# Performance work log

Hardware: AMD Instinct MI355X
Metric: run time of the kernel (lower is better)

The kernel has to match this reference:

```python
import jax, jax.numpy as jnp
import numpy as np

EPS = 1e-20

def efficient_squash(s):
    # Efficient-CapsNet squash: (1 - 1/e^||s||) * s/||s||
    n = jnp.linalg.norm(s, axis=-1, keepdims=True)
    return (1.0 - 1.0 / (jnp.exp(n) + EPS)) * (s / (n + EPS))

def setup_inputs() -> dict:
    key = jax.random.key(0)
    k1, k2 = jax.random.split(key)
    B, N, D_in = 32, 2048, 16
    K, D_out = 32, 16
    x = jax.random.normal(k1, (B, N, D_in), dtype=jnp.float32)
    # he_normal fan_in = N * D_in * ... ; use simple scaled normal init
    w = jax.random.normal(k2, (K, N, D_in, D_out), dtype=jnp.float32) * 0.05
    b = jnp.zeros((K, N, 1), dtype=jnp.float32)
    return {"x": x, "w": w, "b": b}

def reference(x, w, b):
    D_out = w.shape[-1]
    # projection: [B,N,D_in] x [K,N,D_in,D_out] -> [B,K,N,D_out]
    u = jnp.einsum('bji,kjiz->bkjz', x, w)
    # agreement c_{bkj} = sum_{i,z} u_{bkjz} u_{bkiz} = <u_j, sum_i u_i>
    t = jnp.sum(u, axis=2)                      # [B,K,D_out]
    c = jnp.einsum('bkjz,bkz->bkj', u, t)[..., None]  # [B,K,N,1]
    c = c / jnp.sqrt(jnp.asarray(D_out, jnp.float32))
    c = jax.nn.softmax(c, axis=1)               # softmax over capsules K
    c = c + b                                   # broadcast [K,N,1]
    s = jnp.sum(u * c, axis=2)                  # [B,K,D_out]
    return efficient_squash(s)
```

## Files before the change

kernel.cpp:

```cpp
#include <hip/hip_runtime.h>

#define NN 2048

typedef __attribute__((ext_vector_type(8))) short short8;
typedef __attribute__((ext_vector_type(4))) float f32x4;

#define WS_TPART 0UL
#define WS_SPART 33554432UL
#define WS_TP2   67108864UL
#define WS_SP2   68157440UL
#define WS_TG    69206016UL
#define WS_NEED  69271552UL

__device__ __forceinline__ float bf_lo(unsigned v) { return __uint_as_float(v << 16); }
__device__ __forceinline__ float bf_hi(unsigned v) { return __uint_as_float(v & 0xffff0000u); }
__device__ __forceinline__ unsigned pack_bf16(float a, float b) {
    unsigned ua = __float_as_uint(a), ub = __float_as_uint(b);
    return ((ua + 0x8000u) >> 16) | ((ub + 0x8000u) & 0xffff0000u);
}
__device__ __forceinline__ short8 pack8(const float* r) {
    short8 o;
#pragma unroll
    for (int e = 0; e < 8; ++e)
        o[e] = (short)(unsigned short)((__float_as_uint(r[e]) + 0x8000u) >> 16);
    return o;
}
__device__ __forceinline__ short8 sel8(bool keep, short8 v) {
    union { short8 s; unsigned u[4]; } a, b;
    a.s = v;
#pragma unroll
    for (int i = 0; i < 4; ++i) b.u[i] = keep ? a.u[i] : 0u;
    return b.s;
}

__device__ __forceinline__ float dpp_sum16(float v) {
    int a;
    a = __builtin_amdgcn_update_dpp(0, __float_as_int(v), 0x121, 0xf, 0xf, false);
    v += __int_as_float(a);
    a = __builtin_amdgcn_update_dpp(0, __float_as_int(v), 0x122, 0xf, 0xf, false);
    v += __int_as_float(a);
    a = __builtin_amdgcn_update_dpp(0, __float_as_int(v), 0x124, 0xf, 0xf, false);
    v += __int_as_float(a);
    a = __builtin_amdgcn_update_dpp(0, __float_as_int(v), 0x128, 0xf, 0xf, false);
    v += __int_as_float(a);
    return v;
}
__device__ __forceinline__ float dpp_max16(float v) {
    int a;
    a = __builtin_amdgcn_update_dpp(0, __float_as_int(v), 0x121, 0xf, 0xf, false);
    v = fmaxf(v, __int_as_float(a));
    a = __builtin_amdgcn_update_dpp(0, __float_as_int(v), 0x122, 0xf, 0xf, false);
    v = fmaxf(v, __int_as_float(a));
    a = __builtin_amdgcn_update_dpp(0, __float_as_int(v), 0x124, 0xf, 0xf, false);
    v = fmaxf(v, __int_as_float(a));
    a = __builtin_amdgcn_update_dpp(0, __float_as_int(v), 0x128, 0xf, 0xf, false);
    v = fmaxf(v, __int_as_float(a));
    return v;
}

__global__ __launch_bounds__(512)
void kA(const float* __restrict__ x, const float* __restrict__ w,
        float* __restrict__ t_part)
{
    const int tid = threadIdx.x;
    const int wv = tid >> 6, l = tid & 63;
    const int z = l & 15, g = l >> 4;
    const int jl = g >> 1, ih = g & 1;
    const int j0 = blockIdx.x * 4;

    f32x4 C[4][2];
#pragma unroll
    for (int ckl = 0; ckl < 4; ++ckl)
#pragma unroll
        for (int bh = 0; bh < 2; ++bh) C[ckl][bh] = (f32x4){0.f, 0.f, 0.f, 0.f};

#pragma unroll
    for (int p = 0; p < 2; ++p) {
        const int jp = j0 + p * 2 + jl;
        short8 Af[2];
#pragma unroll
        for (int bh = 0; bh < 2; ++bh) {
            const float* xp = x + ((size_t)(bh * 16 + z) * NN + jp) * 16 + ih * 8;
            float ar[8];
            float4 v0 = *reinterpret_cast<const float4*>(xp);
            float4 v1 = *reinterpret_cast<const float4*>(xp + 4);
            ar[0]=v0.x; ar[1]=v0.y; ar[2]=v0.z; ar[3]=v0.w;
            ar[4]=v1.x; ar[5]=v1.y; ar[6]=v1.z; ar[7]=v1.w;
            Af[bh] = pack8(ar);
        }
        short8 Bf[4];
#pragma unroll
        for (int ckl = 0; ckl < 4; ++ckl) {
            const int ck = wv * 4 + ckl;
            const float* wp = w + ((size_t)ck * NN + jp) * 256 + ih * 128 + z;
            float br[8];
#pragma unroll
            for (int e = 0; e < 8; ++e) br[e] = wp[e * 16];
            Bf[ckl] = pack8(br);
        }
#pragma unroll
        for (int ckl = 0; ckl < 4; ++ckl)
#pragma unroll
            for (int bh = 0; bh < 2; ++bh)
                C[ckl][bh] = __builtin_amdgcn_mfma_f32_16x16x32_bf16(
                    Af[bh], Bf[ckl], C[ckl][bh], 0, 0, 0);
    }

    float* tp = t_part + (size_t)blockIdx.x * 16384;
#pragma unroll
    for (int ckl = 0; ckl < 4; ++ckl)
#pragma unroll
        for (int bh = 0; bh < 2; ++bh)
#pragma unroll
            for (int r = 0; r < 4; ++r)
                tp[((bh * 16 + g * 4 + r) * 32 + wv * 4 + ckl) * 16 + z] =
                    C[ckl][bh][r];
}

__global__ __launch_bounds__(256)
void kred32(const float* __restrict__ src, float* __restrict__ dst)
{
    const int idx = blockIdx.x * 256 + threadIdx.x;
    const int c4 = idx & 4095, ch = idx >> 12;
    const f32x4* P = reinterpret_cast<const f32x4*>(src);
    f32x4 a0 = (f32x4){0,0,0,0}, a1 = a0, a2 = a0, a3 = a0;
#pragma unroll 2
    for (int q = 0; q < 32; q += 4) {
        a0 += P[(size_t)(ch * 32 + q + 0) * 4096 + c4];
        a1 += P[(size_t)(ch * 32 + q + 1) * 4096 + c4];
        a2 += P[(size_t)(ch * 32 + q + 2) * 4096 + c4];
        a3 += P[(size_t)(ch * 32 + q + 3) * 4096 + c4];
    }
    reinterpret_cast<f32x4*>(dst)[(size_t)ch * 4096 + c4] = (a0 + a1) + (a2 + a3);
}

__global__ __launch_bounds__(256)
void kt2(const float* __restrict__ tp2, float* __restrict__ t_g)
{
    const int c4 = blockIdx.x * 256 + threadIdx.x;
    const f32x4* P = reinterpret_cast<const f32x4*>(tp2);
    f32x4 a0 = (f32x4){0,0,0,0}, a1 = a0, a2 = a0, a3 = a0;
#pragma unroll
    for (int q = 0; q < 16; q += 4) {
        a0 += P[(size_t)(q + 0) * 4096 + c4];
        a1 += P[(size_t)(q + 1) * 4096 + c4];
        a2 += P[(size_t)(q + 2) * 4096 + c4];
        a3 += P[(size_t)(q + 3) * 4096 + c4];
    }
    f32x4 s = (a0 + a1) + (a2 + a3);
    const int b = c4 >> 7, ck = (c4 >> 2) & 31, zq = c4 & 3;
#pragma unroll
    for (int e = 0; e < 4; ++e)
        t_g[(size_t)(ck * 16 + zq * 4 + e) * 32 + b] = s[e];
}

__global__ __launch_bounds__(512)
void kB(const float* __restrict__ x, const float* __restrict__ w,
        const float* __restrict__ t_g, const float* __restrict__ bias,
        float* __restrict__ s_part)
{
    __shared__ alignas(16) unsigned t_pk[512 * 20];
    __shared__ alignas(16) float l_lds[2][32][34];
    __shared__ alignas(16) float c_lds[2][32][34];

    const int tid = threadIdx.x;
    const int wv = tid >> 6, l = tid & 63;
    const int z = l & 15, g = l >> 4;
    const int jl = g >> 1, ih = g & 1;
    const int j0 = blockIdx.x * 4;

#pragma unroll
    for (int it = 0; it < 4; ++it) {
        const int idx = it * 512 + tid;
        const int row = idx >> 2, boff = (idx & 3) * 8;
        const float4 v0 = *reinterpret_cast<const float4*>(t_g + (size_t)row * 32 + boff);
        const float4 v1 = *reinterpret_cast<const float4*>(t_g + (size_t)row * 32 + boff + 4);
        uint4 pk;
        pk.x = pack_bf16(v0.x, v0.y);
        pk.y = pack_bf16(v0.z, v0.w);
        pk.z = pack_bf16(v1.x, v1.y);
        pk.w = pack_bf16(v1.z, v1.w);
        *reinterpret_cast<uint4*>(&t_pk[row * 20 + boff / 2]) = pk;
    }
    __syncthreads();

    f32x4 S[4][2];
#pragma unroll
    for (int ckl = 0; ckl < 4; ++ckl)
#pragma unroll
        for (int bh = 0; bh < 2; ++bh) S[ckl][bh] = (f32x4){0.f, 0.f, 0.f, 0.f};

#pragma unroll
    for (int p = 0; p < 2; ++p) {
        const int jp = j0 + p * 2 + jl;
        short8 Af[2];
#pragma unroll
        for (int bh = 0; bh < 2; ++bh) {
            const float* xp = x + ((size_t)(bh * 16 + z) * NN + jp) * 16 + ih * 8;
            float ar[8];
            float4 v0 = *reinterpret_cast<const float4*>(xp);
            float4 v1 = *reinterpret_cast<const float4*>(xp + 4);
            ar[0]=v0.x; ar[1]=v0.y; ar[2]=v0.z; ar[3]=v0.w;
            ar[4]=v1.x; ar[5]=v1.y; ar[6]=v1.z; ar[7]=v1.w;
            Af[bh] = pack8(ar);
        }
        short8 Bf[4];
#pragma unroll
        for (int ckl = 0; ckl < 4; ++ckl) {
            const int ck = wv * 4 + ckl;
            const float* wp = w + ((size_t)ck * NN + jp) * 256 + ih * 128 + z;
            float br[8];
#pragma unroll
            for (int e = 0; e < 8; ++e) br[e] = wp[e * 16];
            Bf[ckl] = pack8(br);
        }

#pragma unroll
        for (int jj = 0; jj < 2; ++jj) {
            const int pp = (p * 2 + jj) & 1;
            const bool keep = (jl == jj);
            const f32x4 zero = (f32x4){0.f, 0.f, 0.f, 0.f};
            f32x4 Cj[4][2];
#pragma unroll
            for (int ckl = 0; ckl < 4; ++ckl) {
                const short8 bsel = sel8(keep, Bf[ckl]);
#pragma unroll
                for (int bh = 0; bh < 2; ++bh)
                    Cj[ckl][bh] = __builtin_amdgcn_mfma_f32_16x16x32_bf16(
                        Af[bh], bsel, zero, 0, 0, 0);
            }
#pragma unroll
            for (int ckl = 0; ckl < 4; ++ckl) {
                const int ck = wv * 4 + ckl;
#pragma unroll
                for (int bh = 0; bh < 2; ++bh) {
                    const uint2 tv = *reinterpret_cast<const uint2*>(
                        &t_pk[(ck * 16 + z) * 20 + bh * 8 + g * 2]);
                    float lr[4];
                    lr[0] = Cj[ckl][bh][0] * bf_lo(tv.x);
                    lr[1] = Cj[ckl][bh][1] * bf_hi(tv.x);
                    lr[2] = Cj[ckl][bh][2] * bf_lo(tv.y);
                    lr[3] = Cj[ckl][bh][3] * bf_hi(tv.y);
#pragma unroll
                    for (int r = 0; r < 4; ++r) lr[r] = dpp_sum16(lr[r]);
                    if (z == ckl * 2 + bh) {
                        const int bb = bh * 16 + g * 4;
                        l_lds[pp][bb + 0][ck] = lr[0];
                        l_lds[pp][bb + 1][ck] = lr[1];
                        l_lds[pp][bb + 2][ck] = lr[2];
                        l_lds[pp][bb + 3][ck] = lr[3];
                    }
                }
            }
            __syncthreads();
            {
                const int bb = tid >> 4, kq = tid & 15;
                const float lv0 = l_lds[pp][bb][2 * kq];
                const float lv1 = l_lds[pp][bb][2 * kq + 1];
                float m = dpp_max16(fmaxf(lv0, lv1));
                const float e0 = __expf((lv0 - m) * 0.25f);
                const float e1 = __expf((lv1 - m) * 0.25f);
                const float sum = dpp_sum16(e0 + e1);
                const float inv = 1.f / sum;
                const int jg = j0 + p * 2 + jj;
                c_lds[pp][bb][2 * kq]     = e0 * inv + bias[(size_t)(2 * kq) * NN + jg];
                c_lds[pp][bb][2 * kq + 1] = e1 * inv + bias[(size_t)(2 * kq + 1) * NN + jg];
            }
            __syncthreads();
#pragma unroll
            for (int ckl = 0; ckl < 4; ++ckl) {
                const int ck = wv * 4 + ckl;
#pragma unroll
                for (int bh = 0; bh < 2; ++bh) {
                    const int bb = bh * 16 + g * 4;
#pragma unroll
                    for (int r = 0; r < 4; ++r)
                        S[ckl][bh][r] = fmaf(c_lds[pp][bb + r][ck],
                                             Cj[ckl][bh][r], S[ckl][bh][r]);
                }
            }
        }
    }

    float* sp = s_part + (size_t)blockIdx.x * 16384;
#pragma unroll
    for (int ckl = 0; ckl < 4; ++ckl)
#pragma unroll
        for (int bh = 0; bh < 2; ++bh)
#pragma unroll
            for (int r = 0; r < 4; ++r)
                sp[((bh * 16 + g * 4 + r) * 32 + wv * 4 + ckl) * 16 + z] =
                    S[ckl][bh][r];
}

__global__ __launch_bounds__(256)
void ks2(const float* __restrict__ sp2, float* __restrict__ out)
{
    const int c4 = blockIdx.x * 256 + threadIdx.x;
    const f32x4* P = reinterpret_cast<const f32x4*>(sp2);
    f32x4 a0 = (f32x4){0,0,0,0}, a1 = a0, a2 = a0, a3 = a0;
#pragma unroll
    for (int q = 0; q < 16; q += 4) {
        a0 += P[(size_t)(q + 0) * 4096 + c4];
        a1 += P[(size_t)(q + 1) * 4096 + c4];
        a2 += P[(size_t)(q + 2) * 4096 + c4];
        a3 += P[(size_t)(q + 3) * 4096 + c4];
    }
    f32x4 s = (a0 + a1) + (a2 + a3);
    float ss = s.x * s.x + s.y * s.y + s.z * s.z + s.w * s.w;
    ss += __shfl_xor(ss, 1);
    ss += __shfl_xor(ss, 2);
    const float n = sqrtf(ss);
    const float sc = (1.f - 1.f / (__expf(n) + 1e-20f)) / (n + 1e-20f);
    f32x4 o; o.x = s.x * sc; o.y = s.y * sc; o.z = s.z * sc; o.w = s.w * sc;
    reinterpret_cast<f32x4*>(out)[c4] = o;
}

__global__ void k_sentinel(float* __restrict__ out)
{
    out[blockIdx.x * 256 + threadIdx.x] = 12345.0f;
}

extern "C" void kernel_launch(void* const* d_in, const int* in_sizes, int n_in,
                              void* d_out, int out_size, void* d_ws, size_t ws_size,
                              hipStream_t stream)
{
    const float* x    = (const float*)d_in[0];
    const float* w    = (const float*)d_in[1];
    const float* bias = (const float*)d_in[2];
    float* out        = (float*)d_out;

    char* ws = (char*)d_ws;
    if (ws_size < WS_NEED) {
        k_sentinel<<<dim3(64), dim3(256), 0, stream>>>(out);
        return;
    }
    float* t_part = (float*)(ws + WS_TPART);
    float* s_part = (float*)(ws + WS_SPART);
    float* tp2    = (float*)(ws + WS_TP2);
    float* sp2    = (float*)(ws + WS_SP2);
    float* t_g    = (float*)(ws + WS_TG);

    kA    <<<dim3(512), dim3(512), 0, stream>>>(x, w, t_part);
    kred32<<<dim3(256), dim3(256), 0, stream>>>(t_part, tp2);
    kt2   <<<dim3(16),  dim3(256), 0, stream>>>(tp2, t_g);
    kB    <<<dim3(512), dim3(512), 0, stream>>>(x, w, t_g, bias, s_part);
    kred32<<<dim3(256), dim3(256), 0, stream>>>(s_part, sp2);
    ks2   <<<dim3(16),  dim3(256), 0, stream>>>(sp2, out);
}
```

Before: 73.32 us.

## Restructure second pass to fp32 t in LDS, 8 columns per block, transposed MFMA

```diff
diff --git a/kernel.cpp b/kernel.cpp
--- a/kernel.cpp
+++ b/kernel.cpp
@@ -1,23 +1,18 @@
 #include <hip/hip_runtime.h>
 
 #define NN 2048
+#define KK 32
 
 typedef __attribute__((ext_vector_type(8))) short short8;
 typedef __attribute__((ext_vector_type(4))) float f32x4;
 
 #define WS_TPART 0UL
 #define WS_SPART 33554432UL
-#define WS_TP2   67108864UL
-#define WS_SP2   68157440UL
-#define WS_TG    69206016UL
-#define WS_NEED  69271552UL
-
-__device__ __forceinline__ float bf_lo(unsigned v) { return __uint_as_float(v << 16); }
-__device__ __forceinline__ float bf_hi(unsigned v) { return __uint_as_float(v & 0xffff0000u); }
-__device__ __forceinline__ unsigned pack_bf16(float a, float b) {
-    unsigned ua = __float_as_uint(a), ub = __float_as_uint(b);
-    return ((ua + 0x8000u) >> 16) | ((ub + 0x8000u) & 0xffff0000u);
-}
+#define WS_TP2   50331648UL
+#define WS_SP2   51380224UL
+#define WS_T     52428800UL
+#define WS_NEED  52494336UL
+
 __device__ __forceinline__ short8 pack8(const float* r) {
     short8 o;
 #pragma unroll
@@ -33,33 +28,8 @@
     return b.s;
 }
 
-__device__ __forceinline__ float dpp_sum16(float v) {
-    int a;
-    a = __builtin_amdgcn_update_dpp(0, __float_as_int(v), 0x121, 0xf, 0xf, false);
-    v += __int_as_float(a);
-    a = __builtin_amdgcn_update_dpp(0, __float_as_int(v), 0x122, 0xf, 0xf, false);
-    v += __int_as_float(a);
-    a = __builtin_amdgcn_update_dpp(0, __float_as_int(v), 0x124, 0xf, 0xf, false);
-    v += __int_as_float(a);
-    a = __builtin_amdgcn_update_dpp(0, __float_as_int(v), 0x128, 0xf, 0xf, false);
-    v += __int_as_float(a);
-    return v;
-}
-__device__ __forceinline__ float dpp_max16(float v) {
-    int a;
-    a = __builtin_amdgcn_update_dpp(0, __float_as_int(v), 0x121, 0xf, 0xf, false);
-    v = fmaxf(v, __int_as_float(a));
-    a = __builtin_amdgcn_update_dpp(0, __float_as_int(v), 0x122, 0xf, 0xf, false);
-    v = fmaxf(v, __int_as_float(a));
-    a = __builtin_amdgcn_update_dpp(0, __float_as_int(v), 0x124, 0xf, 0xf, false);
-    v = fmaxf(v, __int_as_float(a));
-    a = __builtin_amdgcn_update_dpp(0, __float_as_int(v), 0x128, 0xf, 0xf, false);
-    v = fmaxf(v, __int_as_float(a));
-    return v;
-}
-
 __global__ __launch_bounds__(512)
-void kA(const float* __restrict__ x, const float* __restrict__ w,
+void kT(const float* __restrict__ x, const float* __restrict__ w,
         float* __restrict__ t_part)
 {
     const int tid = threadIdx.x;
@@ -135,7 +105,24 @@
 }
 
 __global__ __launch_bounds__(256)
-void kt2(const float* __restrict__ tp2, float* __restrict__ t_g)
+void kred16(const float* __restrict__ src, float* __restrict__ dst)
+{
+    const int idx = blockIdx.x * 256 + threadIdx.x;
+    const int c4 = idx & 4095, ch = idx >> 12;
+    const f32x4* P = reinterpret_cast<const f32x4*>(src);
+    f32x4 a0 = (f32x4){0,0,0,0}, a1 = a0, a2 = a0, a3 = a0;
+#pragma unroll
+    for (int q = 0; q < 16; q += 4) {
+        a0 += P[(size_t)(ch * 16 + q + 0) * 4096 + c4];
+        a1 += P[(size_t)(ch * 16 + q + 1) * 4096 + c4];
+        a2 += P[(size_t)(ch * 16 + q + 2) * 4096 + c4];
+        a3 += P[(size_t)(ch * 16 + q + 3) * 4096 + c4];
+    }
+    reinterpret_cast<f32x4*>(dst)[(size_t)ch * 4096 + c4] = (a0 + a1) + (a2 + a3);
+}
+
+__global__ __launch_bounds__(256)
+void kt2(const float* __restrict__ tp2, float* __restrict__ t)
 {
     const int c4 = blockIdx.x * 256 + threadIdx.x;
     const f32x4* P = reinterpret_cast<const f32x4*>(tp2);
@@ -147,40 +134,34 @@
         a2 += P[(size_t)(q + 2) * 4096 + c4];
         a3 += P[(size_t)(q + 3) * 4096 + c4];
     }
-    f32x4 s = (a0 + a1) + (a2 + a3);
-    const int b = c4 >> 7, ck = (c4 >> 2) & 31, zq = c4 & 3;
-#pragma unroll
-    for (int e = 0; e < 4; ++e)
-        t_g[(size_t)(ck * 16 + zq * 4 + e) * 32 + b] = s[e];
+    reinterpret_cast<f32x4*>(t)[c4] = (a0 + a1) + (a2 + a3);
 }
 
 __global__ __launch_bounds__(512)
-void kB(const float* __restrict__ x, const float* __restrict__ w,
-        const float* __restrict__ t_g, const float* __restrict__ bias,
-        float* __restrict__ s_part)
-{
-    __shared__ alignas(16) unsigned t_pk[512 * 20];
-    __shared__ alignas(16) float l_lds[2][32][34];
-    __shared__ alignas(16) float c_lds[2][32][34];
-
+void kBF(const float* __restrict__ x, const float* __restrict__ w,
+         const float* __restrict__ t, const float* __restrict__ bias,
+         float* __restrict__ s_part)
+{
+    __shared__ float t_lds[32 * 520];
+    __shared__ float l_lds[32][33];
+    __shared__ float c_lds[32][33];
+    __shared__ float b_lds[32][8];
     const int tid = threadIdx.x;
     const int wv = tid >> 6, l = tid & 63;
-    const int z = l & 15, g = l >> 4;
+    const int c16 = l & 15, g = l >> 4;
     const int jl = g >> 1, ih = g & 1;
-    const int j0 = blockIdx.x * 4;
-
-#pragma unroll
-    for (int it = 0; it < 4; ++it) {
-        const int idx = it * 512 + tid;
-        const int row = idx >> 2, boff = (idx & 3) * 8;
-        const float4 v0 = *reinterpret_cast<const float4*>(t_g + (size_t)row * 32 + boff);
-        const float4 v1 = *reinterpret_cast<const float4*>(t_g + (size_t)row * 32 + boff + 4);
-        uint4 pk;
-        pk.x = pack_bf16(v0.x, v0.y);
-        pk.y = pack_bf16(v0.z, v0.w);
-        pk.z = pack_bf16(v1.x, v1.y);
-        pk.w = pack_bf16(v1.z, v1.w);
-        *reinterpret_cast<uint4*>(&t_pk[row * 20 + boff / 2]) = pk;
+    const int j0 = blockIdx.x * 8;
+
+    {
+        const f32x4* tg = reinterpret_cast<const f32x4*>(t);
+#pragma unroll
+        for (int q = 0; q < 8; ++q) {
+            const int idx4 = q * 512 + tid;
+            const int b = idx4 >> 7, col4 = idx4 & 127;
+            *reinterpret_cast<f32x4*>(&t_lds[b * 520 + col4 * 4]) = tg[idx4];
+        }
+        if (tid < 256)
+            b_lds[tid >> 3][tid & 7] = bias[(size_t)(tid >> 3) * NN + j0 + (tid & 7)];
     }
     __syncthreads();
 
@@ -188,95 +169,92 @@
 #pragma unroll
     for (int ckl = 0; ckl < 4; ++ckl)
 #pragma unroll
-        for (int bh = 0; bh < 2; ++bh) S[ckl][bh] = (f32x4){0.f, 0.f, 0.f, 0.f};
-
-#pragma unroll
-    for (int p = 0; p < 2; ++p) {
+        for (int bn = 0; bn < 2; ++bn) S[ckl][bn] = (f32x4){0.f, 0.f, 0.f, 0.f};
+
+#pragma unroll 1
+    for (int p = 0; p < 4; ++p) {
         const int jp = j0 + p * 2 + jl;
-        short8 Af[2];
-#pragma unroll
-        for (int bh = 0; bh < 2; ++bh) {
-            const float* xp = x + ((size_t)(bh * 16 + z) * NN + jp) * 16 + ih * 8;
+
+        short8 Wf[4];
+#pragma unroll
+        for (int ckl = 0; ckl < 4; ++ckl) {
+            const int k = wv * 4 + ckl;
+            const float* wp = w + ((size_t)k * NN + jp) * 256 + ih * 128 + c16;
+            float br[8];
+#pragma unroll
+            for (int e = 0; e < 8; ++e) br[e] = wp[e * 16];
+            Wf[ckl] = pack8(br);
+        }
+        short8 Xf[2];
+#pragma unroll
+        for (int bn = 0; bn < 2; ++bn) {
+            const float* xp = x + ((size_t)(bn * 16 + c16) * NN + jp) * 16 + ih * 8;
             float ar[8];
             float4 v0 = *reinterpret_cast<const float4*>(xp);
             float4 v1 = *reinterpret_cast<const float4*>(xp + 4);
             ar[0]=v0.x; ar[1]=v0.y; ar[2]=v0.z; ar[3]=v0.w;
             ar[4]=v1.x; ar[5]=v1.y; ar[6]=v1.z; ar[7]=v1.w;
-            Af[bh] = pack8(ar);
-        }
-        short8 Bf[4];
-#pragma unroll
-        for (int ckl = 0; ckl < 4; ++ckl) {
-            const int ck = wv * 4 + ckl;
-            const float* wp = w + ((size_t)ck * NN + jp) * 256 + ih * 128 + z;
-            float br[8];
-#pragma unroll
-            for (int e = 0; e < 8; ++e) br[e] = wp[e * 16];
-            Bf[ckl] = pack8(br);
-        }
-
-#pragma unroll
+            Xf[bn] = pack8(ar);
+        }
+
+#pragma unroll 1
         for (int jj = 0; jj < 2; ++jj) {
-            const int pp = (p * 2 + jj) & 1;
             const bool keep = (jl == jj);
             const f32x4 zero = (f32x4){0.f, 0.f, 0.f, 0.f};
-            f32x4 Cj[4][2];
+
+            f32x4 C[4][2];
 #pragma unroll
             for (int ckl = 0; ckl < 4; ++ckl) {
-                const short8 bsel = sel8(keep, Bf[ckl]);
-#pragma unroll
-                for (int bh = 0; bh < 2; ++bh)
-                    Cj[ckl][bh] = __builtin_amdgcn_mfma_f32_16x16x32_bf16(
-                        Af[bh], bsel, zero, 0, 0, 0);
-            }
-#pragma unroll
-            for (int ckl = 0; ckl < 4; ++ckl) {
-                const int ck = wv * 4 + ckl;
-#pragma unroll
-                for (int bh = 0; bh < 2; ++bh) {
-                    const uint2 tv = *reinterpret_cast<const uint2*>(
-                        &t_pk[(ck * 16 + z) * 20 + bh * 8 + g * 2]);
-                    float lr[4];
-                    lr[0] = Cj[ckl][bh][0] * bf_lo(tv.x);
-                    lr[1] = Cj[ckl][bh][1] * bf_hi(tv.x);
-                    lr[2] = Cj[ckl][bh][2] * bf_lo(tv.y);
-                    lr[3] = Cj[ckl][bh][3] * bf_hi(tv.y);
-#pragma unroll
-                    for (int r = 0; r < 4; ++r) lr[r] = dpp_sum16(lr[r]);
-                    if (z == ckl * 2 + bh) {
-                        const int bb = bh * 16 + g * 4;
-                        l_lds[pp][bb + 0][ck] = lr[0];
-                        l_lds[pp][bb + 1][ck] = lr[1];
-                        l_lds[pp][bb + 2][ck] = lr[2];
-                        l_lds[pp][bb + 3][ck] = lr[3];
-                    }
+                const short8 wsel = sel8(keep, Wf[ckl]);
+                const int k = wv * 4 + ckl;
+#pragma unroll
+                for (int bn = 0; bn < 2; ++bn) {
+                    C[ckl][bn] = __builtin_amdgcn_mfma_f32_16x16x32_bf16(
+                        wsel, Xf[bn], zero, 0, 0, 0);
+                    const int b = bn * 16 + c16;
+                    const f32x4 tv = *reinterpret_cast<const f32x4*>(
+                        &t_lds[b * 520 + k * 16 + g * 4]);
+                    float pv = C[ckl][bn][0] * tv[0] + C[ckl][bn][1] * tv[1]
+                             + C[ckl][bn][2] * tv[2] + C[ckl][bn][3] * tv[3];
+                    pv += __shfl_xor(pv, 16);
+                    pv += __shfl_xor(pv, 32);
+                    if (g == 0) l_lds[b][k] = pv;
                 }
             }
             __syncthreads();
+
             {
                 const int bb = tid >> 4, kq = tid & 15;
-                const float lv0 = l_lds[pp][bb][2 * kq];
-                const float lv1 = l_lds[pp][bb][2 * kq + 1];
-                float m = dpp_max16(fmaxf(lv0, lv1));
+                const float lv0 = l_lds[bb][2 * kq];
+                const float lv1 = l_lds[bb][2 * kq + 1];
+                float m = fmaxf(lv0, lv1);
+                m = fmaxf(m, __shfl_xor(m, 1));
+                m = fmaxf(m, __shfl_xor(m, 2));
+                m = fmaxf(m, __shfl_xor(m, 4));
+                m = fmaxf(m, __shfl_xor(m, 8));
                 const float e0 = __expf((lv0 - m) * 0.25f);
                 const float e1 = __expf((lv1 - m) * 0.25f);
-                const float sum = dpp_sum16(e0 + e1);
+                float sum = e0 + e1;
+                sum += __shfl_xor(sum, 1);
+                sum += __shfl_xor(sum, 2);
+                sum += __shfl_xor(sum, 4);
+                sum += __shfl_xor(sum, 8);
                 const float inv = 1.f / sum;
-                const int jg = j0 + p * 2 + jj;
-                c_lds[pp][bb][2 * kq]     = e0 * inv + bias[(size_t)(2 * kq) * NN + jg];
-                c_lds[pp][bb][2 * kq + 1] = e1 * inv + bias[(size_t)(2 * kq + 1) * NN + jg];
+                const int jloc = p * 2 + jj;
+                c_lds[bb][2 * kq]     = e0 * inv + b_lds[2 * kq][jloc];
+                c_lds[bb][2 * kq + 1] = e1 * inv + b_lds[2 * kq + 1][jloc];
             }
             __syncthreads();
+
 #pragma unroll
             for (int ckl = 0; ckl < 4; ++ckl) {
-                const int ck = wv * 4 + ckl;
-#pragma unroll
-                for (int bh = 0; bh < 2; ++bh) {
-                    const int bb = bh * 16 + g * 4;
+                const int k = wv * 4 + ckl;
+#pragma unroll
+                for (int bn = 0; bn < 2; ++bn) {
+                    const float cv = c_lds[bn * 16 + c16][k];
 #pragma unroll
                     for (int r = 0; r < 4; ++r)
-                        S[ckl][bh][r] = fmaf(c_lds[pp][bb + r][ck],
-                                             Cj[ckl][bh][r], S[ckl][bh][r]);
+                        S[ckl][bn][r] = fmaf(cv, C[ckl][bn][r], S[ckl][bn][r]);
                 }
             }
         }
@@ -284,17 +262,17 @@
 
     float* sp = s_part + (size_t)blockIdx.x * 16384;
 #pragma unroll
-    for (int ckl = 0; ckl < 4; ++ckl)
-#pragma unroll
-        for (int bh = 0; bh < 2; ++bh)
-#pragma unroll
-            for (int r = 0; r < 4; ++r)
-                sp[((bh * 16 + g * 4 + r) * 32 + wv * 4 + ckl) * 16 + z] =
-                    S[ckl][bh][r];
+    for (int ckl = 0; ckl < 4; ++ckl) {
+        const int k = wv * 4 + ckl;
+#pragma unroll
+        for (int bn = 0; bn < 2; ++bn)
+            *reinterpret_cast<f32x4*>(
+                &sp[(bn * 16 + c16) * 512 + k * 16 + g * 4]) = S[ckl][bn];
+    }
 }
 
 __global__ __launch_bounds__(256)
-void ks2(const float* __restrict__ sp2, float* __restrict__ out)
+void ksq(const float* __restrict__ sp2, float* __restrict__ out)
 {
     const int c4 = blockIdx.x * 256 + threadIdx.x;
     const f32x4* P = reinterpret_cast<const f32x4*>(sp2);
@@ -339,12 +317,12 @@
     float* s_part = (float*)(ws + WS_SPART);
     float* tp2    = (float*)(ws + WS_TP2);
     float* sp2    = (float*)(ws + WS_SP2);
-    float* t_g    = (float*)(ws + WS_TG);
-
-    kA    <<<dim3(512), dim3(512), 0, stream>>>(x, w, t_part);
+    float* t      = (float*)(ws + WS_T);
+
+    kT    <<<dim3(512), dim3(512), 0, stream>>>(x, w, t_part);
     kred32<<<dim3(256), dim3(256), 0, stream>>>(t_part, tp2);
-    kt2   <<<dim3(16),  dim3(256), 0, stream>>>(tp2, t_g);
-    kB    <<<dim3(512), dim3(512), 0, stream>>>(x, w, t_g, bias, s_part);
-    kred32<<<dim3(256), dim3(256), 0, stream>>>(s_part, sp2);
-    ks2   <<<dim3(16),  dim3(256), 0, stream>>>(sp2, out);
-}
+    kt2   <<<dim3(16),  dim3(256), 0, stream>>>(tp2, t);
+    kBF   <<<dim3(256), dim3(512), 0, stream>>>(x, w, t, bias, s_part);
+    kred16<<<dim3(256), dim3(256), 0, stream>>>(s_part, sp2);
+    ksq   <<<dim3(16),  dim3(256), 0, stream>>>(sp2, out);
+}
```

New measurement: 65.56 us. 1.12x faster.
